# Optimization experiments

Hardware: AMD Instinct MI355X
Metric: run time of the kernel (lower is better)

The kernel has to match this reference:

```python
import jax, jax.numpy as jnp
import numpy as np

EMBED_DIM = 1024
N_HEAD = 16

def setup_inputs() -> dict:
    key = jax.random.key(0)
    ks = jax.random.split(key, 5)
    C = EMBED_DIM
    x = jax.random.normal(ks[0], (2, 2048, C), dtype=jnp.float32)
    s = 1.0 / np.sqrt(C)
    W_attn = jax.random.normal(ks[1], (C, 3 * C), dtype=jnp.float32) * s
    b_attn = jnp.zeros((3 * C,), dtype=jnp.float32)
    W_proj = jax.random.normal(ks[2], (C, C), dtype=jnp.float32) * s
    b_proj = jnp.zeros((C,), dtype=jnp.float32)
    return {"x": x, "W_attn": W_attn, "b_attn": b_attn, "W_proj": W_proj, "b_proj": b_proj}

def reference(x, W_attn, b_attn, W_proj, b_proj):
    B, T, C = x.shape
    H = N_HEAD
    D = C // H
    qkv = x @ W_attn + b_attn                      # [B,T,3C]
    q, k, v = jnp.split(qkv, 3, axis=-1)
    # [B,H,T,D]
    q = q.reshape(B, T, H, D).transpose(0, 2, 1, 3)
    k = k.reshape(B, T, H, D).transpose(0, 2, 1, 3)
    v = v.reshape(B, T, H, D).transpose(0, 2, 1, 3)
    att = jnp.einsum('bhqd,bhkd->bhqk', q, k) * (1.0 / jnp.sqrt(jnp.asarray(D, x.dtype)))
    causal = jnp.tril(jnp.ones((T, T), dtype=bool))
    att = jnp.where(causal, att, -jnp.inf)
    att = jax.nn.softmax(att, axis=-1)
    y = jnp.einsum('bhqk,bhkd->bhqd', att, v)      # [B,H,T,D]
    y = y.transpose(0, 2, 1, 3).reshape(B, T, C)
    return y @ W_proj + b_proj
```

## Files before the change

kernel.cpp:

```cpp
#include <hip/hip_runtime.h>
#include <stdint.h>

typedef __attribute__((ext_vector_type(4))) float f32x4;
typedef __attribute__((ext_vector_type(8))) __bf16 bf16x8;
typedef __attribute__((ext_vector_type(8))) unsigned short u16x8;

__device__ __forceinline__ unsigned short f2b(float f) {
  unsigned u = __float_as_uint(f);
  u += 0x7FFFu + ((u >> 16) & 1u);
  return (unsigned short)(u >> 16);
}
__device__ __forceinline__ float b2f(unsigned short s) {
  unsigned u = (unsigned)s << 16;
  return __uint_as_float(u);
}
__device__ __forceinline__ unsigned cvtpk_bf16(float lo, float hi) {
  unsigned r;
  asm("v_cvt_pk_bf16_f32 %0, %1, %2" : "=v"(r) : "v"(lo), "v"(hi));
  return r;
}

__device__ __forceinline__ void gload_lds16(const void* g, void* l) {
  typedef __attribute__((address_space(1))) void GV1;
  typedef __attribute__((address_space(3))) void LV3;
  __builtin_amdgcn_global_load_lds((GV1*)(void*)g, (LV3*)l, 16, 0, 0);
}

__global__ __launch_bounds__(256) void convert_f32_bf16(const float* __restrict__ in,
                                                        unsigned short* __restrict__ out, int n) {
  int i = (blockIdx.x * 256 + threadIdx.x) * 8;
  if (i >= n) return;
  float4 a = *(const float4*)(in + i);
  float4 b = *(const float4*)(in + i + 4);
  u16x8 r;
  r[0] = f2b(a.x); r[1] = f2b(a.y); r[2] = f2b(a.z); r[3] = f2b(a.w);
  r[4] = f2b(b.x); r[5] = f2b(b.y); r[6] = f2b(b.z); r[7] = f2b(b.w);
  *(u16x8*)(out + i) = r;
}

__global__ __launch_bounds__(256) void transpose_f32_bf16(const float* __restrict__ W,
                                                          unsigned short* __restrict__ Wt,
                                                          int K, int N) {
  __shared__ unsigned short tile[32][33];
  int n0 = blockIdx.x * 32, k0 = blockIdx.y * 32;
  int tx = threadIdx.x, ty = threadIdx.y;
  #pragma unroll
  for (int j = 0; j < 32; j += 8)
    tile[ty + j][tx] = f2b(W[(size_t)(k0 + ty + j) * N + n0 + tx]);
  __syncthreads();
  #pragma unroll
  for (int j = 0; j < 32; j += 8)
    Wt[(size_t)(n0 + ty + j) * K + k0 + tx] = tile[tx][ty + j];
}

template <bool OUT_BF16, bool VSPLIT>
__global__ __launch_bounds__(512) void gemm_bt(const unsigned short* __restrict__ A,
                                               const unsigned short* __restrict__ Bt,
                                               const float* __restrict__ bias,
                                               void* __restrict__ Cout,
                                               unsigned short* __restrict__ vT,
                                               int M, int N, int K) {
  __shared__ unsigned short SMEM[32768];
  const int m0 = blockIdx.x * 128, n0 = blockIdx.y * 128;
  const int tid = threadIdx.x;
  const int w = tid >> 6, l = tid & 63;
  const int wm = w >> 2, wn = w & 3;
  const int c = l & 15, g = l >> 4;
  const int NT = K >> 6;
  const unsigned short* aptr[2];
  const unsigned short* bptr[2];
  #pragma unroll
  for (int i = 0; i < 2; ++i) {
    int rb = w * 16 + i * 8;
    aptr[i] = A  + (size_t)(m0 + rb + (l >> 3)) * K + (l & 7) * 8;
    bptr[i] = Bt + (size_t)(n0 + rb + (l >> 3)) * K + (l & 7) * 8;
  }
  f32x4 acc[4][2] = {};
  #pragma unroll
  for (int i = 0; i < 2; ++i) {
    int rb = w * 16 + i * 8;
    gload_lds16(aptr[i], &SMEM[rb * 64]);
    gload_lds16(bptr[i], &SMEM[8192 + rb * 64]);
  }
  __syncthreads();
  for (int t = 0; t < NT; ++t) {
    const int cur = t & 1;
    const unsigned short* Ab = &SMEM[cur * 16384];
    const unsigned short* Bb = &SMEM[cur * 16384 + 8192];
    if (t + 1 < NT) {
      unsigned short* An = &SMEM[(cur ^ 1) * 16384];
      unsigned short* Bn = &SMEM[(cur ^ 1) * 16384 + 8192];
      #pragma unroll
      for (int i = 0; i < 2; ++i) {
        int rb = w * 16 + i * 8;
        gload_lds16(aptr[i] + (size_t)(t + 1) * 64, &An[rb * 64]);
        gload_lds16(bptr[i] + (size_t)(t + 1) * 64, &Bn[rb * 64]);
      }
    }
    #pragma unroll
    for (int ks = 0; ks < 2; ++ks) {
      bf16x8 af[4], bf[2];
      #pragma unroll
      for (int mi = 0; mi < 4; ++mi)
        af[mi] = *(const bf16x8*)&Ab[(wm * 64 + mi * 16 + c) * 64 + ks * 32 + g * 8];
      #pragma unroll
      for (int ni = 0; ni < 2; ++ni)
        bf[ni] = *(const bf16x8*)&Bb[(wn * 32 + ni * 16 + c) * 64 + ks * 32 + g * 8];
      __builtin_amdgcn_s_setprio(1);
      #pragma unroll
      for (int mi = 0; mi < 4; ++mi)
        #pragma unroll
        for (int ni = 0; ni < 2; ++ni)
          acc[mi][ni] = __builtin_amdgcn_mfma_f32_16x16x32_bf16(af[mi], bf[ni], acc[mi][ni], 0, 0, 0);
      __builtin_amdgcn_s_setprio(0);
    }
    __syncthreads();
  }
  if (VSPLIT && n0 >= 2048) {
    unsigned short* TR = SMEM;
    #pragma unroll
    for (int mi = 0; mi < 4; ++mi)
      #pragma unroll
      for (int ni = 0; ni < 2; ++ni) {
        int cl = wn * 32 + ni * 16 + c;
        float bv = bias[n0 + cl];
        int rlb = wm * 64 + mi * 16 + 4 * g;
        ushort4 o4;
        o4.x = f2b(acc[mi][ni][0] + bv); o4.y = f2b(acc[mi][ni][1] + bv);
        o4.z = f2b(acc[mi][ni][2] + bv); o4.w = f2b(acc[mi][ni][3] + bv);
        *(ushort4*)&TR[cl * 136 + rlb] = o4;
      }
    __syncthreads();
    const int d0 = n0 - 2048;
    #pragma unroll
    for (int p = 0; p < 4; ++p) {
      int rowl = p * 32 + (tid >> 4);
      *(u16x8*)(vT + (size_t)(d0 + rowl) * 4096 + m0 + (tid & 15) * 8) =
          *(const u16x8*)&TR[rowl * 136 + (tid & 15) * 8];
    }
    return;
  }
  const int NS = VSPLIT ? 2048 : N;
  #pragma unroll
  for (int mi = 0; mi < 4; ++mi) {
    #pragma unroll
    for (int ni = 0; ni < 2; ++ni) {
      int colg = n0 + wn * 32 + ni * 16 + c;
      float bv = bias[colg];
      #pragma unroll
      for (int r = 0; r < 4; ++r) {
        int rowg = m0 + wm * 64 + mi * 16 + 4 * g + r;
        float v = acc[mi][ni][r] + bv;
        if (OUT_BF16)
          ((unsigned short*)Cout)[(size_t)rowg * NS + colg] = f2b(v);
        else
          ((float*)Cout)[(size_t)rowg * NS + colg] = v;
      }
    }
  }
}

__global__ __launch_bounds__(512) void attn_kernel(const unsigned short* __restrict__ qk,
                                                   const unsigned short* __restrict__ vT,
                                                   unsigned short* __restrict__ partO,
                                                   float* __restrict__ partML) {
  __shared__ unsigned short K_lds[2][64 * 64];
  __shared__ unsigned short V_lds[2][64 * 64];
  const int bid = blockIdx.x;
  const int bh = bid & 31;
  const int cid = 39 - (bid >> 5);
  int qt, ct;
  if (cid < 4)       { qt = cid;            ct = 0; }
  else if (cid < 12) { int e = cid - 4;  qt = 4 + (e >> 1);  ct = e & 1; }
  else if (cid < 24) { int e = cid - 12; int q3 = e / 3; qt = 8 + q3; ct = e - 3 * q3; }
  else               { int e = cid - 24; qt = 12 + (e >> 2); ct = e & 3; }
  const int ntt = 2 * qt + 2;
  const int t0 = ct * 8;
  const int ntl = min(ntt - t0, 8);
  const int b = bh >> 4, h = bh & 15;
  const int tid = threadIdx.x, w = tid >> 6, l = tid & 63;
  const int c = l & 15, g = l >> 4;
  const int hi = g >> 1;
  const int srcA = c + ((g & 1) << 5);
  const int srcB = srcA + 16;
  const size_t row0 = (size_t)b * 2048;
  const float SCL = 0.18033688f;
  const int KSTRIDE = 64 * 2048;
  const int VSTRIDE = 64;

  const int q0w = qt * 128 + w * 16;
  const int qg = q0w + c;

  bf16x8 qf[2];
  #pragma unroll
  for (int ks = 0; ks < 2; ++ks)
    qf[ks] = *(const bf16x8*)(qk + (row0 + qg) * 2048 + h * 64 + ks * 32 + g * 8);

  f32x4 acc[4] = {};
  float mstate = -1e30f, lstate = 0.f;

  const int krow = w * 8 + (l >> 3);
  const int kch = (l & 7) ^ (krow & 7);
  const unsigned short* kptr = qk + (row0 + t0 * 64 + krow) * 2048 + 1024 + h * 64 + kch * 8;
  const unsigned short* vptr = vT + (size_t)(h * 64 + krow) * 4096 + (b * 2048 + t0 * 64) + kch * 8;
  const int kdst = (w * 8) * 64;

  gload_lds16(kptr, &K_lds[0][kdst]);
  gload_lds16(vptr, &V_lds[0][kdst]);
  __syncthreads();

  for (int lt = 0; lt < ntl; ++lt) {
    const int cur = lt & 1;
    const int kv0 = (t0 + lt) * 64;
    const bool pre = (lt + 1 < ntl);
    if (pre) {
      gload_lds16(kptr + KSTRIDE, &K_lds[cur ^ 1][kdst]);
      gload_lds16(vptr + VSTRIDE, &V_lds[cur ^ 1][kdst]);
    }
    kptr += KSTRIDE;
    vptr += VSTRIDE;
    if (kv0 <= q0w + 15) {
      const char* Kb = (const char*)K_lds[cur];
      const char* Vb = (const char*)V_lds[cur];
      f32x4 s[4] = {};
      #pragma unroll
      for (int ks = 0; ks < 2; ++ks) {
        bf16x8 kf[4];
        #pragma unroll
        for (int nk = 0; nk < 4; ++nk) {
          int row = nk * 16 + c;
          kf[nk] = *(const bf16x8*)(Kb + row * 128 + ((ks * 64 + g * 16) ^ ((row & 7) << 4)));
        }
        __builtin_amdgcn_s_setprio(1);
        #pragma unroll
        for (int nk = 0; nk < 4; ++nk)
          s[nk] = __builtin_amdgcn_mfma_f32_16x16x32_bf16(kf[nk], qf[ks], s[nk], 0, 0, 0);
        __builtin_amdgcn_s_setprio(0);
      }
      if (kv0 + 63 > q0w) {
        #pragma unroll
        for (int nk = 0; nk < 4; ++nk)
          #pragma unroll
          for (int r = 0; r < 4; ++r) {
            int kvg = kv0 + nk * 16 + 4 * g + r;
            if (kvg > qg) s[nk][r] = -1e30f;
          }
      }
      float a0 = fmaxf(fmaxf(s[0][0], s[0][1]), fmaxf(s[0][2], s[0][3]));
      float a1 = fmaxf(fmaxf(s[1][0], s[1][1]), fmaxf(s[1][2], s[1][3]));
      float a2 = fmaxf(fmaxf(s[2][0], s[2][1]), fmaxf(s[2][2], s[2][3]));
      float a3 = fmaxf(fmaxf(s[3][0], s[3][1]), fmaxf(s[3][2], s[3][3]));
      float mx = fmaxf(fmaxf(a0, a1), fmaxf(a2, a3));
      mx = fmaxf(mx, __shfl_xor(mx, 16));
      mx = fmaxf(mx, __shfl_xor(mx, 32));
      if (!__all(mx <= mstate)) {
        float mnew = fmaxf(mstate, mx);
        float alpha = exp2f((mstate - mnew) * SCL);
        mstate = mnew;
        lstate *= alpha;
        #pragma unroll
        for (int nd = 0; nd < 4; ++nd) acc[nd] *= alpha;
      }
      float ms = mstate * SCL;
      #pragma unroll
      for (int nk = 0; nk < 4; ++nk) {
        #pragma unroll
        for (int r = 0; r < 4; ++r) s[nk][r] = exp2f(fmaf(s[nk][r], SCL, -ms));
        lstate += (s[nk][0] + s[nk][1]) + (s[nk][2] + s[nk][3]);
      }
      unsigned pk[4][2];
      #pragma unroll
      for (int nk = 0; nk < 4; ++nk) {
        pk[nk][0] = cvtpk_bf16(s[nk][0], s[nk][1]);
        pk[nk][1] = cvtpk_bf16(s[nk][2], s[nk][3]);
      }
      #pragma unroll
      for (int vks = 0; vks < 2; ++vks) {
        unsigned rA00 = __shfl(pk[2 * vks][0], srcA, 64);
        unsigned rA01 = __shfl(pk[2 * vks][1], srcA, 64);
        unsigned rA10 = __shfl(pk[2 * vks + 1][0], srcA, 64);
        unsigned rA11 = __shfl(pk[2 * vks + 1][1], srcA, 64);
        unsigned rB00 = __shfl(pk[2 * vks][0], srcB, 64);
        unsigned rB01 = __shfl(pk[2 * vks][1], srcB, 64);
        unsigned rB10 = __shfl(pk[2 * vks + 1][0], srcB, 64);
        unsigned rB11 = __shfl(pk[2 * vks + 1][1], srcB, 64);
        union { unsigned u[4]; bf16x8 v; } pa;
        pa.u[0] = hi ? rA10 : rA00;
        pa.u[1] = hi ? rA11 : rA01;
        pa.u[2] = hi ? rB10 : rB00;
        pa.u[3] = hi ? rB11 : rB01;
        bf16x8 vf[4];
        #pragma unroll
        for (int nd = 0; nd < 4; ++nd) {
          int row = nd * 16 + c;
          vf[nd] = *(const bf16x8*)(Vb + row * 128 + ((vks * 64 + g * 16) ^ ((row & 7) << 4)));
        }
        __builtin_amdgcn_s_setprio(1);
        #pragma unroll
        for (int nd = 0; nd < 4; ++nd)
          acc[nd] = __builtin_amdgcn_mfma_f32_16x16x32_bf16(vf[nd], pa.v, acc[nd], 0, 0, 0);
        __builtin_amdgcn_s_setprio(0);
      }
    }
    __syncthreads();
  }

  float lsum = lstate;
  lsum += __shfl_xor(lsum, 16);
  lsum += __shfl_xor(lsum, 32);
  const int qrow = w * 16 + c;
  #pragma unroll
  for (int nd = 0; nd < 4; ++nd) {
    ushort4 o4;
    o4.x = f2b(acc[nd][0]); o4.y = f2b(acc[nd][1]);
    o4.z = f2b(acc[nd][2]); o4.w = f2b(acc[nd][3]);
    *(ushort4*)(partO + (size_t)bid * 8192 + qrow * 64 + nd * 16 + 4 * g) = o4;
  }
  if (g == 0) {
    partML[(size_t)bid * 256 + qrow * 2 + 0] = mstate;
    partML[(size_t)bid * 256 + qrow * 2 + 1] = lsum;
  }
}

__global__ __launch_bounds__(256) void attn_combine(const unsigned short* __restrict__ partO,
                                                    const float* __restrict__ partML,
                                                    unsigned short* __restrict__ out) {
  const int bid = blockIdx.x;
  const int qt = bid >> 5, bh = bid & 31;
  const int b = bh >> 4, h = bh & 15;
  const int np = (2 * qt + 9) >> 3;
  const int base = (qt < 4) ? qt
                 : (qt < 8) ? 4 + 2 * (qt - 4)
                 : (qt < 12) ? 12 + 3 * (qt - 8)
                 : 24 + 4 * (qt - 12);
  const int t = threadIdx.x;
  const int row = t >> 1, cg = (t & 1) * 32;
  const float SCL = 0.18033688f;
  float mstar = -1e30f;
  #pragma unroll
  for (int p = 0; p < 4; ++p)
    if (p < np)
      mstar = fmaxf(mstar, partML[(size_t)(((39 - (base + p)) << 5) | bh) * 256 + row * 2]);
  float L = 0.f;
  float o[32];
  #pragma unroll
  for (int j = 0; j < 32; ++j) o[j] = 0.f;
  #pragma unroll
  for (int p = 0; p < 4; ++p) {
    if (p < np) {
      int slot = ((39 - (base + p)) << 5) | bh;
      float mp = partML[(size_t)slot * 256 + row * 2 + 0];
      float lp = partML[(size_t)slot * 256 + row * 2 + 1];
      float wgt = exp2f((mp - mstar) * SCL);
      L = fmaf(wgt, lp, L);
      const unsigned short* src = partO + (size_t)slot * 8192 + row * 64 + cg;
      #pragma unroll
      for (int q = 0; q < 4; ++q) {
        u16x8 a = *(const u16x8*)(src + q * 8);
        #pragma unroll
        for (int j = 0; j < 8; ++j)
          o[q * 8 + j] = fmaf(b2f(a[j]), wgt, o[q * 8 + j]);
      }
    }
  }
  float rinv = 1.0f / L;
  size_t trow = (size_t)b * 2048 + qt * 128 + row;
  #pragma unroll
  for (int q = 0; q < 4; ++q) {
    u16x8 r;
    #pragma unroll
    for (int j = 0; j < 8; ++j) r[j] = f2b(o[q * 8 + j] * rinv);
    *(u16x8*)(out + trow * 1024 + h * 64 + cg + q * 8) = r;
  }
}

extern "C" void kernel_launch(void* const* d_in, const int* in_sizes, int n_in,
                              void* d_out, int out_size, void* d_ws, size_t ws_size,
                              hipStream_t stream) {
  const float* x      = (const float*)d_in[0];
  const float* W_attn = (const float*)d_in[1];
  const float* b_attn = (const float*)d_in[2];
  const float* W_proj = (const float*)d_in[3];
  const float* b_proj = (const float*)d_in[4];
  float* out = (float*)d_out;

  char* ws = (char*)d_ws;
  unsigned short* Wproj_t  = (unsigned short*)(ws + 0);
  unsigned short* qk       = (unsigned short*)(ws + 2097152);
  unsigned short* vT       = (unsigned short*)(ws + 18874368);
  unsigned short* x_bf     = (unsigned short*)(ws + 27262976);
  unsigned short* Wattn_t  = (unsigned short*)(ws + 35651584);
  unsigned short* partO    = (unsigned short*)(ws + 27262976);
  unsigned short* attn_out = (unsigned short*)(ws + 48234496);
  float*          partML   = (float*)(ws + 56623104);

  convert_f32_bf16<<<2048, 256, 0, stream>>>(x, x_bf, 4194304);
  transpose_f32_bf16<<<dim3(96, 32), dim3(32, 8), 0, stream>>>(W_attn, Wattn_t, 1024, 3072);
  transpose_f32_bf16<<<dim3(32, 32), dim3(32, 8), 0, stream>>>(W_proj, Wproj_t, 1024, 1024);

  gemm_bt<true, true><<<dim3(32, 24), 512, 0, stream>>>(x_bf, Wattn_t, b_attn, qk, vT,
                                                        4096, 3072, 1024);
  attn_kernel<<<1280, 512, 0, stream>>>(qk, vT, partO, partML);
  attn_combine<<<512, 256, 0, stream>>>(partO, partML, attn_out);
  gemm_bt<false, false><<<dim3(32, 8), 512, 0, stream>>>(attn_out, Wproj_t, b_proj, out, nullptr,
                                                         4096, 1024, 1024);
}
```

Measured before the change: 137.1 us.

## Triple-buffer K/V tiles in attention with partial vmcnt waits

Result: no change. 137.9 us (+0.6%).

```diff
diff --git a/kernel.cpp b/kernel.cpp
--- a/kernel.cpp
+++ b/kernel.cpp
@@ -24,6 +24,19 @@
   typedef __attribute__((address_space(1))) void GV1;
   typedef __attribute__((address_space(3))) void LV3;
   __builtin_amdgcn_global_load_lds((GV1*)(void*)g, (LV3*)l, 16, 0, 0);
+}
+
+__device__ __forceinline__ void tile_barrier_keep2() {
+  asm volatile("s_waitcnt vmcnt(2)" ::: "memory");
+  __builtin_amdgcn_sched_barrier(0);
+  __builtin_amdgcn_s_barrier();
+  __builtin_amdgcn_sched_barrier(0);
+}
+__device__ __forceinline__ void tile_barrier_keep0() {
+  asm volatile("s_waitcnt vmcnt(0)" ::: "memory");
+  __builtin_amdgcn_sched_barrier(0);
+  __builtin_amdgcn_s_barrier();
+  __builtin_amdgcn_sched_barrier(0);
 }
 
 __global__ __launch_bounds__(256) void convert_f32_bf16(const float* __restrict__ in,
@@ -164,8 +177,8 @@
                                                    const unsigned short* __restrict__ vT,
                                                    unsigned short* __restrict__ partO,
                                                    float* __restrict__ partML) {
-  __shared__ unsigned short K_lds[2][64 * 64];
-  __shared__ unsigned short V_lds[2][64 * 64];
+  __shared__ unsigned short K_lds[3][64 * 64];
+  __shared__ unsigned short V_lds[3][64 * 64];
   const int bid = blockIdx.x;
   const int bh = bid & 31;
   const int cid = 39 - (bid >> 5);
@@ -207,15 +220,22 @@
 
   gload_lds16(kptr, &K_lds[0][kdst]);
   gload_lds16(vptr, &V_lds[0][kdst]);
-  __syncthreads();
-
+  if (ntl > 1) {
+    gload_lds16(kptr + KSTRIDE, &K_lds[1][kdst]);
+    gload_lds16(vptr + VSTRIDE, &V_lds[1][kdst]);
+    tile_barrier_keep2();
+  } else {
+    tile_barrier_keep0();
+  }
+
+  int cur = 0;
   for (int lt = 0; lt < ntl; ++lt) {
-    const int cur = lt & 1;
     const int kv0 = (t0 + lt) * 64;
-    const bool pre = (lt + 1 < ntl);
-    if (pre) {
-      gload_lds16(kptr + KSTRIDE, &K_lds[cur ^ 1][kdst]);
-      gload_lds16(vptr + VSTRIDE, &V_lds[cur ^ 1][kdst]);
+    const bool pre2 = (lt + 2 < ntl);
+    if (pre2) {
+      int sb = cur + 2; if (sb >= 3) sb -= 3;
+      gload_lds16(kptr + 2 * KSTRIDE, &K_lds[sb][kdst]);
+      gload_lds16(vptr + 2 * VSTRIDE, &V_lds[sb][kdst]);
     }
     kptr += KSTRIDE;
     vptr += VSTRIDE;
@@ -302,7 +322,11 @@
         __builtin_amdgcn_s_setprio(0);
       }
     }
-    __syncthreads();
+    if (lt + 1 < ntl) {
+      if (pre2) tile_barrier_keep2();
+      else      tile_barrier_keep0();
+    }
+    cur = (cur + 1 == 3) ? 0 : cur + 1;
   }
 
   float lsum = lstate;
```
